# Kernel tuning notes

Measured on AMD Instinct MI355X. Metric: run time of the kernel, lower is better.

The kernel has to match this reference:

```python
import jax, jax.numpy as jnp
import numpy as np
import math

INNER = 96
EPS = 1e-8  # torch CosineSimilarity eps


def _proj(x, W1, W2):
    # nn.Linear(C,C,bias=False) -> ReLU -> nn.Linear(C,inner,bias=False)
    return jax.nn.relu(x @ W1) @ W2


def _cos(a, b):
    # torch CosineSimilarity(dim=-1): dot / (max(||a||,eps)*max(||b||,eps))
    num = jnp.sum(a * b, axis=-1)
    na = jnp.maximum(jnp.linalg.norm(a, axis=-1), EPS)
    nb = jnp.maximum(jnp.linalg.norm(b, axis=-1), EPS)
    return num / (na * nb)


def setup_inputs() -> dict:
    key = jax.random.key(0)
    ks = jax.random.split(key, 8)
    B, C, H, W = 128, 768, 7, 7
    sc1 = 1.0 / math.sqrt(C)
    inp = {
        "features_a": jax.random.normal(ks[0], (B, C, H, W), jnp.float32),
        "features_b": jax.random.normal(ks[1], (B, C, H, W), jnp.float32),
        "Wq1": jax.random.normal(ks[2], (C, C), jnp.float32) * sc1,
        "Wq2": jax.random.normal(ks[3], (C, INNER), jnp.float32) * sc1,
        "Wk1": jax.random.normal(ks[4], (C, C), jnp.float32) * sc1,
        "Wk2": jax.random.normal(ks[5], (C, INNER), jnp.float32) * sc1,
        "Wv1": jax.random.normal(ks[6], (C, C), jnp.float32) * sc1,
        "Wv2": jax.random.normal(ks[7], (C, INNER), jnp.float32) * sc1,
    }
    return inp


def reference(features_a, features_b, Wq1, Wq2, Wk1, Wk2, Wv1, Wv2):
    B, C = features_a.shape[0], features_a.shape[1]
    # [B, C, H, W] -> [B, S, C]
    fa = features_a.reshape(B, C, -1).transpose(0, 2, 1)
    fb = features_b.reshape(features_b.shape[0], C, -1).transpose(0, 2, 1)

    qa, ka, va = _proj(fa, Wq1, Wq2), _proj(fa, Wk1, Wk2), _proj(fa, Wv1, Wv2)
    qb, kb, vb = _proj(fb, Wq1, Wq2), _proj(fb, Wk1, Wk2), _proj(fb, Wv1, Wv2)

    scale = 1.0 / math.sqrt(INNER)

    # query_b vs key_a: [Bb, Ba, Sq, Sk]
    scores_ba = jnp.einsum('bqe,ake->baqk', qb, ka) * scale
    probs_ba = jax.nn.softmax(scores_ba, axis=-1)
    aligned_a = jnp.einsum('baqk,ake->baqe', probs_ba, va)  # [Bb, Ba, S, inner]

    # query_a vs key_b: [Bb, Ba, Sq, Sk]
    scores_ab = jnp.einsum('aqe,bke->baqk', qa, kb) * scale
    probs_ab = jax.nn.softmax(scores_ab, axis=-1)
    aligned_b = jnp.einsum('baqk,bke->baqe', probs_ab, vb)  # [Bb, Ba, S, inner]

    sim = _cos(va[None, :, :, :], aligned_b) + _cos(vb[:, None, :, :], aligned_a)
    return sim.mean(-1)  # [Bb, Ba]
```

## Files before the change

kernel.cpp:

```cpp
#include <hip/hip_runtime.h>
#include <hip/hip_bf16.h>
#include <math.h>

typedef __attribute__((ext_vector_type(8))) short bf16x8;
typedef __attribute__((ext_vector_type(4))) float f32x4;

#define MROWS 12544
#define CDIM 768
#define INNER 96
#define S49 49
#define NSIDE 6272
#define SCALE 0.10206207261596577f
#define SCALE_EXP2 ((float)(0.10206207261596577 * 1.4426950408889634))

__device__ __forceinline__ unsigned short f2bf(float f) {
  union { float f; unsigned u; } v; v.f = f;
  unsigned u = v.u;
  return (unsigned short)((u + 0x7fffu + ((u >> 16) & 1u)) >> 16);
}
__device__ __forceinline__ float bf2f(unsigned short h) {
  union { unsigned u; float f; } v; v.u = ((unsigned)h) << 16;
  return v.f;
}
__device__ __forceinline__ unsigned pack_bf16_rn(float a, float b) {
  union { float f; unsigned u; } ua, ub; ua.f = a; ub.f = b;
  return __builtin_amdgcn_perm(ub.u + 0x8000u, ua.u + 0x8000u, 0x07060302u);
}

__device__ __forceinline__ void gld16(const unsigned short* g, unsigned short* l) {
  __builtin_amdgcn_global_load_lds(
      (const __attribute__((address_space(1))) unsigned int*)(g),
      (__attribute__((address_space(3))) unsigned int*)(l), 16, 0, 0);
}

__global__ __launch_bounds__(256) void prep_all(
    const float* __restrict__ fa, const float* __restrict__ fb,
    const float* __restrict__ w10, const float* __restrict__ w11,
    const float* __restrict__ w12, const float* __restrict__ w20,
    const float* __restrict__ w21, const float* __restrict__ w22,
    unsigned short* __restrict__ X,
    unsigned short* __restrict__ W1T, unsigned short* __restrict__ W2T,
    unsigned short* __restrict__ VtKpad) {
  const int t = threadIdx.x;
  int id = blockIdx.x;
  if (id < 3072) {
    __shared__ float T[64][50];
    const int z = id / 1536; id -= z * 1536;
    const int ct = id % 12, img = id / 12;
    const float* feat = z ? fb : fa;
    const float* src = feat + (size_t)img * (CDIM * S49) + (size_t)ct * 64 * S49;
    for (int idx = t; idx < 64 * S49; idx += 256) {
      int cc = idx / S49, s = idx - cc * S49;
      T[cc][s] = src[cc * S49 + s];
    }
    __syncthreads();
    unsigned short* dst = X + (size_t)(z * 128 + img) * S49 * CDIM + ct * 64;
    for (int idx = t; idx < S49 * 64; idx += 256) {
      int s = idx >> 6, cc = idx & 63;
      dst[(size_t)s * CDIM + cc] = f2bf(T[cc][s]);
    }
  } else if (id < 5016) {
    __shared__ float T[32][33];
    id -= 3072;
    const float* src;
    unsigned short* dst;
    int C, ctile, rtile;
    if (id < 1728) {
      int wdx = id / 576, tid = id - wdx * 576;
      ctile = tid % 24; rtile = tid / 24;
      src = wdx == 0 ? w10 : (wdx == 1 ? w11 : w12);
      dst = W1T + (size_t)wdx * CDIM * CDIM;
      C = CDIM;
    } else {
      id -= 1728;
      int wdx = id / 72, tid = id - wdx * 72;
      ctile = tid % 3; rtile = tid / 3;
      src = wdx == 0 ? w20 : (wdx == 1 ? w21 : w22);
      dst = W2T + (size_t)wdx * INNER * CDIM;
      C = INNER;
    }
    const int c0 = ctile * 32, r0 = rtile * 32;
    for (int idx = t; idx < 1024; idx += 256) {
      int rr = idx >> 5, cc = idx & 31;
      T[rr][cc] = src[(size_t)(r0 + rr) * C + c0 + cc];
    }
    __syncthreads();
    for (int idx = t; idx < 1024; idx += 256) {
      int rr = idx >> 5, cc = idx & 31;
      dst[(size_t)(c0 + rr) * CDIM + r0 + cc] = f2bf(T[cc][rr]);
    }
  } else {
    id -= 5016;
    ushort4* p4 = (ushort4*)VtKpad;
    const ushort4 z = make_ushort4(0, 0, 0, 0);
#pragma unroll
    for (int i = 0; i < 32; i++)
      p4[(size_t)id * 8192 + i * 256 + t] = z;
  }
}

__global__ __launch_bounds__(256) void gemm1b3(const unsigned short* __restrict__ X,
                                               const unsigned short* __restrict__ W1T,
                                               unsigned short* __restrict__ H,
                                               int wbase, int hsel) {
  __shared__ __align__(16) unsigned short As[128 * 64];
  __shared__ __align__(16) unsigned short Bs[128 * 64];
  const int t = threadIdx.x;
  const int lane = t & 63, w = t >> 6;
  const int lr = lane & 15, lq = lane >> 4;
  const int wm = w & 1, wn = w >> 1;
  const int m0 = blockIdx.y * 128, n0 = blockIdx.x * 128;
  const int wdx = blockIdx.z + wbase;
  const unsigned short* W1w = W1T + (size_t)wdx * CDIM * CDIM;
  unsigned short* Hw = H + (hsel ? (size_t)wdx * MROWS * CDIM : 0);
  const f32x4 z4 = {0.f, 0.f, 0.f, 0.f};
  f32x4 acc[4][4] = {{z4, z4, z4, z4}, {z4, z4, z4, z4},
                     {z4, z4, z4, z4}, {z4, z4, z4, z4}};

  for (int k0 = 0; k0 < CDIM; k0 += 64) {
    __syncthreads();
#pragma unroll
    for (int j = 0; j < 4; j++) {
      int idx = t + j * 256;
      int row = idx >> 3, col = (idx & 7) * 8;
      gld16(X + (size_t)(m0 + row) * CDIM + k0 + col, As + idx * 8);
      gld16(W1w + (size_t)(n0 + row) * CDIM + k0 + col, Bs + idx * 8);
    }
    __syncthreads();
#pragma unroll
    for (int ks = 0; ks < 2; ks++) {
      bf16x8 a[4], b[4];
#pragma unroll
      for (int mt = 0; mt < 4; mt++)
        a[mt] = *(const bf16x8*)(As + (wm * 64 + mt * 16 + lr) * 64 + ks * 32 + lq * 8);
#pragma unroll
      for (int nt = 0; nt < 4; nt++)
        b[nt] = *(const bf16x8*)(Bs + (wn * 64 + nt * 16 + lr) * 64 + ks * 32 + lq * 8);
#pragma unroll
      for (int mt = 0; mt < 4; mt++)
#pragma unroll
        for (int nt = 0; nt < 4; nt++)
          acc[mt][nt] = __builtin_amdgcn_mfma_f32_16x16x32_bf16(a[mt], b[nt], acc[mt][nt], 0, 0, 0);
    }
  }
#pragma unroll
  for (int mt = 0; mt < 4; mt++)
#pragma unroll
    for (int nt = 0; nt < 4; nt++)
#pragma unroll
      for (int r = 0; r < 4; r++) {
        int m = m0 + wm * 64 + mt * 16 + lq * 4 + r;
        int n = n0 + wn * 64 + nt * 16 + lr;
        Hw[(size_t)m * CDIM + n] = f2bf(fmaxf(acc[mt][nt][r], 0.f));
      }
}

#define LDK 72
__global__ __launch_bounds__(256) void gemm2b3(const unsigned short* __restrict__ H,
                                               const unsigned short* __restrict__ W2T,
                                               unsigned short* __restrict__ QKV,
                                               unsigned short* __restrict__ Kpad,
                                               unsigned short* __restrict__ Vt,
                                               float* __restrict__ vnorm,
                                               int wbase, int hsel) {
  __shared__ __align__(16) unsigned short As[64 * LDK];
  __shared__ __align__(16) unsigned short Bs[96 * LDK];
  const int t = threadIdx.x;
  const int lane = t & 63, w = t >> 6;
  const int lr = lane & 15, lq = lane >> 4;
  const int m0 = blockIdx.x * 64;
  const int wdx = blockIdx.y + wbase;
  const unsigned short* Hw = H + (hsel ? (size_t)wdx * MROWS * CDIM : 0);
  const unsigned short* W2w = W2T + (size_t)wdx * INNER * CDIM;
  const f32x4 z4 = {0.f, 0.f, 0.f, 0.f};
  f32x4 acc[6] = {z4, z4, z4, z4, z4, z4};

  for (int k0 = 0; k0 < CDIM; k0 += 64) {
    __syncthreads();
    for (int c = t; c < 512; c += 256) {
      int r = c >> 3, kc = (c & 7) * 8;
      *(uint4*)(As + r * LDK + kc) = *(const uint4*)(Hw + (size_t)(m0 + r) * CDIM + k0 + kc);
    }
    for (int c = t; c < 768; c += 256) {
      int r = c >> 3, kc = (c & 7) * 8;
      *(uint4*)(Bs + r * LDK + kc) = *(const uint4*)(W2w + (size_t)r * CDIM + k0 + kc);
    }
    __syncthreads();
#pragma unroll
    for (int kk = 0; kk < 2; kk++) {
      bf16x8 a = *(const bf16x8*)(As + (w * 16 + lr) * LDK + kk * 32 + lq * 8);
#pragma unroll
      for (int nt = 0; nt < 6; nt++) {
        bf16x8 b = *(const bf16x8*)(Bs + (nt * 16 + lr) * LDK + kk * 32 + lq * 8);
        acc[nt] = __builtin_amdgcn_mfma_f32_16x16x32_bf16(a, b, acc[nt], 0, 0, 0);
      }
    }
  }
  float nsq[4] = {0.f, 0.f, 0.f, 0.f};
#pragma unroll
  for (int nt = 0; nt < 6; nt++)
#pragma unroll
    for (int r = 0; r < 4; r++) {
      int m = m0 + w * 16 + lq * 4 + r;
      int e = nt * 16 + lr;
      float v = acc[nt][r];
      int img = m / 49, s = m - img * 49;
      if (wdx == 0) {
        QKV[(size_t)m * INNER + e] = f2bf(v * SCALE_EXP2);
      } else if (wdx == 1) {
        Kpad[(size_t)(img * 64 + s) * INNER + e] = f2bf(v);
      } else {
        QKV[(size_t)(2 * MROWS + m) * INNER + e] = f2bf(v);
        Vt[(size_t)img * (INNER * 64) + e * 64 + s] = f2bf(v);
        nsq[r] += v * v;
      }
    }
  if (wdx == 2) {
#pragma unroll
    for (int r = 0; r < 4; r++) {
      float p = nsq[r];
      p += __shfl_xor(p, 1, 16);
      p += __shfl_xor(p, 2, 16);
      p += __shfl_xor(p, 4, 16);
      p += __shfl_xor(p, 8, 16);
      if (lr == 0) vnorm[m0 + w * 16 + lq * 4 + r] = sqrtf(p);
    }
  }
}

#define LVS 72
__global__ __launch_bounds__(256) void attn8(const unsigned short* __restrict__ Qp,
                                             const unsigned short* __restrict__ Kpad,
                                             const unsigned short* __restrict__ V,
                                             const unsigned short* __restrict__ Vt,
                                             const float* __restrict__ vnorm,
                                             float* __restrict__ cosbuf) {
  __shared__ __align__(16) unsigned short KsD[2][64 * INNER];
  __shared__ __align__(16) unsigned short VtD[2][INNER * 64];
  __shared__ __align__(16) unsigned short Ps[4][32 * LVS];

  const int t = threadIdx.x;
  const int lane = t & 63, w = t >> 6;
  const int lr = lane & 15, lq = lane >> 4;
  const f32x4 z4 = {0.f, 0.f, 0.f, 0.f};

  int bx = blockIdx.x;
  const int dir = bx / 392; bx -= dir * 392;
  const int chunk = bx >> 3, fg = bx & 7;
  const int r0 = chunk * 128;
  const int qbase = dir * NSIDE;

  int goK[3], goV[3], lo[3];
#pragma unroll
  for (int j = 0; j < 3; j++) {
    int l = (w * 3 + j) * 64 + lane;
    lo[j] = l * 8;
    int rK = l / 12, scK = l - rK * 12;
    int ccK = scK - ((rK >> 1) & 7); if (ccK < 0) ccK += 12;
    goK[j] = rK * INNER + ccK * 8;
    int rV = l >> 3, scV = l & 7;
    int ccV = (scV - (rV & 7)) & 7;
    goV[j] = rV * 64 + ccV * 8;
  }
  int rdK[3], rdV[2];
#pragma unroll
  for (int ks = 0; ks < 3; ks++) {
    int sc = (ks * 4 + lq + ((lr >> 1) & 7)) % 12;
    rdK[ks] = lr * INNER + sc * 8;
  }
#pragma unroll
  for (int ks = 0; ks < 2; ks++) {
    int sc = (ks * 4 + lq + (lr & 7)) & 7;
    rdV[ks] = lr * 64 + sc * 8;
  }

  bf16x8 qf[2][3];
#pragma unroll
  for (int qt = 0; qt < 2; qt++) {
    const int qrow = qbase + r0 + w * 32 + qt * 16 + lr;
#pragma unroll
    for (int ks = 0; ks < 3; ks++)
      qf[qt][ks] = *(const bf16x8*)(Qp + (size_t)qrow * INNER + ks * 32 + lq * 8);
  }
  float rv[2][6][4], invvn[2];
#pragma unroll
  for (int qt = 0; qt < 2; qt++) {
    const int qrow = qbase + r0 + w * 32 + qt * 16 + lr;
    invvn[qt] = 1.f / fmaxf(vnorm[qrow], 1e-8f);
#pragma unroll
    for (int et = 0; et < 6; et++) {
      ushort4 u = *(const ushort4*)(V + (size_t)qrow * INNER + et * 16 + lq * 4);
      rv[qt][et][0] = bf2f(u.x); rv[qt][et][1] = bf2f(u.y);
      rv[qt][et][2] = bf2f(u.z); rv[qt][et][3] = bf2f(u.w);
    }
  }

  unsigned short* Pw = &Ps[w][0];
  const int kimg0 = (dir == 0 ? 128 : 0) + fg * 16;
  {
    const unsigned short* kg = Kpad + (size_t)kimg0 * (64 * INNER);
    const unsigned short* vg = Vt + (size_t)kimg0 * (INNER * 64);
#pragma unroll
    for (int j = 0; j < 3; j++) {
      gld16(kg + goK[j], &KsD[0][0] + lo[j]);
      gld16(vg + goV[j], &VtD[0][0] + lo[j]);
    }
  }
  for (int fi = 0; fi < 16; fi++) {
    const int f = fg * 16 + fi;
    __syncthreads();
    if (fi < 15) {
      const unsigned short* kg = Kpad + (size_t)(kimg0 + fi + 1) * (64 * INNER);
      const unsigned short* vg = Vt + (size_t)(kimg0 + fi + 1) * (INNER * 64);
      unsigned short* kd = &KsD[1 - (fi & 1)][0];
      unsigned short* vd = &VtD[1 - (fi & 1)][0];
#pragma unroll
      for (int j = 0; j < 3; j++) {
        gld16(kg + goK[j], kd + lo[j]);
        gld16(vg + goV[j], vd + lo[j]);
      }
    }
    const unsigned short* KsC = &KsD[fi & 1][0];
    const unsigned short* VtC = &VtD[fi & 1][0];
    f32x4 s4[2][4] = {{z4, z4, z4, z4}, {z4, z4, z4, z4}};
#pragma unroll
    for (int ks = 0; ks < 3; ks++) {
#pragma unroll
      for (int kt = 0; kt < 4; kt++) {
        bf16x8 a = *(const bf16x8*)(KsC + kt * (16 * INNER) + rdK[ks]);
        s4[0][kt] = __builtin_amdgcn_mfma_f32_16x16x32_bf16(a, qf[0][ks], s4[0][kt], 0, 0, 0);
        s4[1][kt] = __builtin_amdgcn_mfma_f32_16x16x32_bf16(a, qf[1][ks], s4[1][kt], 0, 0, 0);
      }
    }
#pragma unroll
    for (int qt = 0; qt < 2; qt++)
#pragma unroll
      for (int kt = 0; kt < 4; kt++) {
        float e0 = __builtin_exp2f(s4[qt][kt][0]);
        float e1 = __builtin_exp2f(s4[qt][kt][1]);
        float e2 = __builtin_exp2f(s4[qt][kt][2]);
        float e3 = __builtin_exp2f(s4[qt][kt][3]);
        uint2 pk = make_uint2(pack_bf16_rn(e0, e1), pack_bf16_rn(e2, e3));
        *(uint2*)(Pw + (qt * 16 + lr) * LVS + kt * 16 + lq * 4) = pk;
      }
    f32x4 pv[2][6] = {{z4, z4, z4, z4, z4, z4}, {z4, z4, z4, z4, z4, z4}};
#pragma unroll
    for (int ks = 0; ks < 2; ks++) {
      bf16x8 b0 = *(const bf16x8*)(Pw + (0 * 16 + lr) * LVS + ks * 32 + lq * 8);
      bf16x8 b1 = *(const bf16x8*)(Pw + (1 * 16 + lr) * LVS + ks * 32 + lq * 8);
#pragma unroll
      for (int et = 0; et < 6; et++) {
        bf16x8 a = *(const bf16x8*)(VtC + et * (16 * 64) + rdV[ks]);
        pv[0][et] = __builtin_amdgcn_mfma_f32_16x16x32_bf16(a, b0, pv[0][et], 0, 0, 0);
        pv[1][et] = __builtin_amdgcn_mfma_f32_16x16x32_bf16(a, b1, pv[1][et], 0, 0, 0);
      }
    }
#pragma unroll
    for (int qt = 0; qt < 2; qt++) {
      float d = 0.f, nn = 0.f;
#pragma unroll
      for (int et = 0; et < 6; et++)
#pragma unroll
        for (int r = 0; r < 4; r++) {
          float al = pv[qt][et][r];
          d += al * rv[qt][et][r];
          nn += al * al;
        }
      d += __shfl_xor(d, 16, 64);  d += __shfl_xor(d, 32, 64);
      nn += __shfl_xor(nn, 16, 64); nn += __shfl_xor(nn, 32, 64);
      if (lane < 16) {
        float cv = d * __frsqrt_rn(fmaxf(nn, 1e-40f)) * invvn[qt];
        cosbuf[(size_t)(dir * 128 + f) * NSIDE + r0 + w * 32 + qt * 16 + lr] = cv;
      }
    }
  }
}

__global__ __launch_bounds__(256) void reduce_out(const float* __restrict__ cosbuf,
                                                  float* __restrict__ out) {
  const int t = threadIdx.x, lane = t & 63, wv = t >> 6;
  const int pair = blockIdx.x * 4 + wv;
  const int bb = pair >> 7, aa = pair & 127;
  float v = 0.f;
  if (lane < S49) {
    v  = cosbuf[(size_t)bb * NSIDE + aa * S49 + lane];
    v += cosbuf[(size_t)(128 + aa) * NSIDE + bb * S49 + lane];
  }
  for (int m = 1; m < 64; m <<= 1) v += __shfl_xor(v, m, 64);
  if (lane == 0) out[pair] = v * (1.f / 49.f);
}

extern "C" void kernel_launch(void* const* d_in, const int* in_sizes, int n_in,
                              void* d_out, int out_size, void* d_ws, size_t ws_size,
                              hipStream_t stream) {
  const float* fa  = (const float*)d_in[0];
  const float* fb  = (const float*)d_in[1];
  const float* W1[3] = {(const float*)d_in[2], (const float*)d_in[4], (const float*)d_in[6]};
  const float* W2[3] = {(const float*)d_in[3], (const float*)d_in[5], (const float*)d_in[7]};
  float* out = (float*)d_out;

  unsigned short* p = (unsigned short*)d_ws;
  unsigned short* Xbf = p;                 p += (size_t)MROWS * CDIM;
  unsigned short* W1T = p;                 p += (size_t)3 * CDIM * CDIM;
  unsigned short* W2T = p;                 p += (size_t)3 * INNER * CDIM;
  unsigned short* QKV = p;                 p += (size_t)3 * MROWS * INNER;
  unsigned short* Vt  = p;                 p += (size_t)256 * INNER * 64;
  unsigned short* Kpad = p;                p += (size_t)256 * 64 * INNER;
  float* vnorm = (float*)p;                p += (size_t)MROWS * 2;
  float* cosbuf = (float*)p;               p += (size_t)256 * NSIDE * 2;
  unsigned short* H = p;                   p += (size_t)3 * MROWS * CDIM;
  const size_t need_batched = (size_t)(p - (unsigned short*)d_ws) * 2;
  const int batched = ws_size >= need_batched;

  prep_all<<<dim3(5112), 256, 0, stream>>>(fa, fb, W1[0], W1[1], W1[2],
                                           W2[0], W2[1], W2[2],
                                           Xbf, W1T, W2T, Vt );
  if (batched) {
    gemm1b3<<<dim3(CDIM / 128, MROWS / 128, 3), 256, 0, stream>>>(Xbf, W1T, H, 0, 1);
    gemm2b3<<<dim3(MROWS / 64, 3), 256, 0, stream>>>(H, W2T, QKV, Kpad, Vt, vnorm, 0, 1);
  } else {
    for (int wdx = 0; wdx < 3; wdx++) {
      gemm1b3<<<dim3(CDIM / 128, MROWS / 128, 1), 256, 0, stream>>>(Xbf, W1T, H, wdx, 0);
      gemm2b3<<<dim3(MROWS / 64, 1), 256, 0, stream>>>(H, W2T, QKV, Kpad, Vt, vnorm, wdx, 0);
    }
  }
  attn8<<<dim3(2 * 392), 256, 0, stream>>>(
      QKV, Kpad, QKV + (size_t)2 * MROWS * INNER, Vt, vnorm, cosbuf);
  reduce_out<<<dim3(4096), 256, 0, stream>>>(cosbuf, out);
}
```

Measured before the change: 306.3 us.

## Widen gemm1 to 512 threads and cut attention LDS with single V buffer and swizzled P

The first projection GEMM now runs 8 waves per 128x128 tile, each owning a 32x64 sub-tile, which halves accumulator registers per thread and adds waves for latency hiding. The attention kernel drops V double-buffering: V is loaded into a single LDS buffer at the start of each iteration, and the next K tile is prefetched after an extra barrier placed mid-iteration. The P staging buffer loses its row padding and uses an XOR swizzle to avoid bank conflicts. Together these lower LDS use to raise occupancy, at the cost of an extra barrier and V loads that are less overlapped with compute.

```diff
diff --git a/kernel.cpp b/kernel.cpp
--- a/kernel.cpp
+++ b/kernel.cpp
@@ -99,7 +99,7 @@
   }
 }
 
-__global__ __launch_bounds__(256) void gemm1b3(const unsigned short* __restrict__ X,
+__global__ __launch_bounds__(512) void gemm1b4(const unsigned short* __restrict__ X,
                                                const unsigned short* __restrict__ W1T,
                                                unsigned short* __restrict__ H,
                                                int wbase, int hsel) {
@@ -108,20 +108,20 @@
   const int t = threadIdx.x;
   const int lane = t & 63, w = t >> 6;
   const int lr = lane & 15, lq = lane >> 4;
-  const int wm = w & 1, wn = w >> 1;
+  const int wm = w & 3;
+  const int wn = w >> 2;
   const int m0 = blockIdx.y * 128, n0 = blockIdx.x * 128;
   const int wdx = blockIdx.z + wbase;
   const unsigned short* W1w = W1T + (size_t)wdx * CDIM * CDIM;
   unsigned short* Hw = H + (hsel ? (size_t)wdx * MROWS * CDIM : 0);
   const f32x4 z4 = {0.f, 0.f, 0.f, 0.f};
-  f32x4 acc[4][4] = {{z4, z4, z4, z4}, {z4, z4, z4, z4},
-                     {z4, z4, z4, z4}, {z4, z4, z4, z4}};
+  f32x4 acc[2][4] = {{z4, z4, z4, z4}, {z4, z4, z4, z4}};
 
   for (int k0 = 0; k0 < CDIM; k0 += 64) {
     __syncthreads();
 #pragma unroll
-    for (int j = 0; j < 4; j++) {
-      int idx = t + j * 256;
+    for (int j = 0; j < 2; j++) {
+      int idx = t + j * 512;
       int row = idx >> 3, col = (idx & 7) * 8;
       gld16(X + (size_t)(m0 + row) * CDIM + k0 + col, As + idx * 8);
       gld16(W1w + (size_t)(n0 + row) * CDIM + k0 + col, Bs + idx * 8);
@@ -129,27 +129,27 @@
     __syncthreads();
 #pragma unroll
     for (int ks = 0; ks < 2; ks++) {
-      bf16x8 a[4], b[4];
-#pragma unroll
-      for (int mt = 0; mt < 4; mt++)
-        a[mt] = *(const bf16x8*)(As + (wm * 64 + mt * 16 + lr) * 64 + ks * 32 + lq * 8);
+      bf16x8 a[2], b[4];
+#pragma unroll
+      for (int mt = 0; mt < 2; mt++)
+        a[mt] = *(const bf16x8*)(As + (wm * 32 + mt * 16 + lr) * 64 + ks * 32 + lq * 8);
 #pragma unroll
       for (int nt = 0; nt < 4; nt++)
         b[nt] = *(const bf16x8*)(Bs + (wn * 64 + nt * 16 + lr) * 64 + ks * 32 + lq * 8);
 #pragma unroll
-      for (int mt = 0; mt < 4; mt++)
+      for (int mt = 0; mt < 2; mt++)
 #pragma unroll
         for (int nt = 0; nt < 4; nt++)
           acc[mt][nt] = __builtin_amdgcn_mfma_f32_16x16x32_bf16(a[mt], b[nt], acc[mt][nt], 0, 0, 0);
     }
   }
 #pragma unroll
-  for (int mt = 0; mt < 4; mt++)
+  for (int mt = 0; mt < 2; mt++)
 #pragma unroll
     for (int nt = 0; nt < 4; nt++)
 #pragma unroll
       for (int r = 0; r < 4; r++) {
-        int m = m0 + wm * 64 + mt * 16 + lq * 4 + r;
+        int m = m0 + wm * 32 + mt * 16 + lq * 4 + r;
         int n = n0 + wn * 64 + nt * 16 + lr;
         Hw[(size_t)m * CDIM + n] = f2bf(fmaxf(acc[mt][nt][r], 0.f));
       }
@@ -228,16 +228,15 @@
   }
 }
 
-#define LVS 72
-__global__ __launch_bounds__(256) void attn8(const unsigned short* __restrict__ Qp,
+__global__ __launch_bounds__(256) void attn9(const unsigned short* __restrict__ Qp,
                                              const unsigned short* __restrict__ Kpad,
                                              const unsigned short* __restrict__ V,
                                              const unsigned short* __restrict__ Vt,
                                              const float* __restrict__ vnorm,
                                              float* __restrict__ cosbuf) {
   __shared__ __align__(16) unsigned short KsD[2][64 * INNER];
-  __shared__ __align__(16) unsigned short VtD[2][INNER * 64];
-  __shared__ __align__(16) unsigned short Ps[4][32 * LVS];
+  __shared__ __align__(16) unsigned short VtS[INNER * 64];
+  __shared__ __align__(16) unsigned short Ps[4][32 * 64];
 
   const int t = threadIdx.x;
   const int lane = t & 63, w = t >> 6;
@@ -299,29 +298,18 @@
   const int kimg0 = (dir == 0 ? 128 : 0) + fg * 16;
   {
     const unsigned short* kg = Kpad + (size_t)kimg0 * (64 * INNER);
-    const unsigned short* vg = Vt + (size_t)kimg0 * (INNER * 64);
-#pragma unroll
-    for (int j = 0; j < 3; j++) {
-      gld16(kg + goK[j], &KsD[0][0] + lo[j]);
-      gld16(vg + goV[j], &VtD[0][0] + lo[j]);
-    }
+#pragma unroll
+    for (int j = 0; j < 3; j++) gld16(kg + goK[j], &KsD[0][0] + lo[j]);
   }
   for (int fi = 0; fi < 16; fi++) {
     const int f = fg * 16 + fi;
     __syncthreads();
-    if (fi < 15) {
-      const unsigned short* kg = Kpad + (size_t)(kimg0 + fi + 1) * (64 * INNER);
-      const unsigned short* vg = Vt + (size_t)(kimg0 + fi + 1) * (INNER * 64);
-      unsigned short* kd = &KsD[1 - (fi & 1)][0];
-      unsigned short* vd = &VtD[1 - (fi & 1)][0];
-#pragma unroll
-      for (int j = 0; j < 3; j++) {
-        gld16(kg + goK[j], kd + lo[j]);
-        gld16(vg + goV[j], vd + lo[j]);
-      }
+    {
+      const unsigned short* vg = Vt + (size_t)(kimg0 + fi) * (INNER * 64);
+#pragma unroll
+      for (int j = 0; j < 3; j++) gld16(vg + goV[j], VtS + lo[j]);
     }
     const unsigned short* KsC = &KsD[fi & 1][0];
-    const unsigned short* VtC = &VtD[fi & 1][0];
     f32x4 s4[2][4] = {{z4, z4, z4, z4}, {z4, z4, z4, z4}};
 #pragma unroll
     for (int ks = 0; ks < 3; ks++) {
@@ -341,16 +329,28 @@
         float e2 = __builtin_exp2f(s4[qt][kt][2]);
         float e3 = __builtin_exp2f(s4[qt][kt][3]);
         uint2 pk = make_uint2(pack_bf16_rn(e0, e1), pack_bf16_rn(e2, e3));
-        *(uint2*)(Pw + (qt * 16 + lr) * LVS + kt * 16 + lq * 4) = pk;
-      }
+        int row = qt * 16 + lr;
+        int ch = (2 * kt + (lq >> 1)) ^ (row & 7);
+        *(uint2*)(Pw + row * 64 + ch * 8 + (lq & 1) * 4) = pk;
+      }
+    __syncthreads();
+    if (fi < 15) {
+      const unsigned short* kg = Kpad + (size_t)(kimg0 + fi + 1) * (64 * INNER);
+      unsigned short* kd = &KsD[1 - (fi & 1)][0];
+#pragma unroll
+      for (int j = 0; j < 3; j++) gld16(kg + goK[j], kd + lo[j]);
+    }
     f32x4 pv[2][6] = {{z4, z4, z4, z4, z4, z4}, {z4, z4, z4, z4, z4, z4}};
 #pragma unroll
     for (int ks = 0; ks < 2; ks++) {
-      bf16x8 b0 = *(const bf16x8*)(Pw + (0 * 16 + lr) * LVS + ks * 32 + lq * 8);
-      bf16x8 b1 = *(const bf16x8*)(Pw + (1 * 16 + lr) * LVS + ks * 32 + lq * 8);
+      int row0 = 0 * 16 + lr, row1 = 1 * 16 + lr;
+      int ch0 = ((ks * 4 + lq) ^ (row0 & 7));
+      int ch1 = ((ks * 4 + lq) ^ (row1 & 7));
+      bf16x8 b0 = *(const bf16x8*)(Pw + row0 * 64 + ch0 * 8);
+      bf16x8 b1 = *(const bf16x8*)(Pw + row1 * 64 + ch1 * 8);
 #pragma unroll
       for (int et = 0; et < 6; et++) {
-        bf16x8 a = *(const bf16x8*)(VtC + et * (16 * 64) + rdV[ks]);
+        bf16x8 a = *(const bf16x8*)(VtS + et * (16 * 64) + rdV[ks]);
         pv[0][et] = __builtin_amdgcn_mfma_f32_16x16x32_bf16(a, b0, pv[0][et], 0, 0, 0);
         pv[1][et] = __builtin_amdgcn_mfma_f32_16x16x32_bf16(a, b1, pv[1][et], 0, 0, 0);
       }
@@ -416,15 +416,15 @@
                                            W2[0], W2[1], W2[2],
                                            Xbf, W1T, W2T, Vt );
   if (batched) {
-    gemm1b3<<<dim3(CDIM / 128, MROWS / 128, 3), 256, 0, stream>>>(Xbf, W1T, H, 0, 1);
+    gemm1b4<<<dim3(CDIM / 128, MROWS / 128, 3), 512, 0, stream>>>(Xbf, W1T, H, 0, 1);
     gemm2b3<<<dim3(MROWS / 64, 3), 256, 0, stream>>>(H, W2T, QKV, Kpad, Vt, vnorm, 0, 1);
   } else {
     for (int wdx = 0; wdx < 3; wdx++) {
-      gemm1b3<<<dim3(CDIM / 128, MROWS / 128, 1), 256, 0, stream>>>(Xbf, W1T, H, wdx, 0);
+      gemm1b4<<<dim3(CDIM / 128, MROWS / 128, 1), 512, 0, stream>>>(Xbf, W1T, H, wdx, 0);
       gemm2b3<<<dim3(MROWS / 64, 1), 256, 0, stream>>>(H, W2T, QKV, Kpad, Vt, vnorm, wdx, 0);
     }
   }
-  attn8<<<dim3(2 * 392), 256, 0, stream>>>(
+  attn9<<<dim3(2 * 392), 256, 0, stream>>>(
       QKV, Kpad, QKV + (size_t)2 * MROWS * INNER, Vt, vnorm, cosbuf);
   reduce_out<<<dim3(4096), 256, 0, stream>>>(cosbuf, out);
 }
```

After: 304.5 us. Within noise of the previous version (-0.6%).
